# Kernel optimization log

Hardware: AMD Instinct MI355X
Metric: run time of the kernel (lower is better)

## Reference

```python
import jax, jax.numpy as jnp
import numpy as np

B, S, V, E, H = 1024, 64, 32, 256, 512
META = 13


def setup_inputs() -> dict:
    key = jax.random.key(0)
    ks = jax.random.split(key, 12)
    return {
        "image_representation": jax.random.normal(ks[0], (B, META), jnp.float32),
        "messages": jax.random.randint(ks[1], (B, S), 0, V),
        "embedding": jax.random.normal(ks[2], (V, E), jnp.float32) * 0.1,
        "w_ih": jax.random.normal(ks[3], (4 * H, E), jnp.float32) * 0.02,
        "w_hh": jax.random.normal(ks[4], (4 * H, H), jnp.float32) * 0.02,
        "b_ih": jnp.zeros((4 * H,), jnp.float32),
        "b_hh": jnp.zeros((4 * H,), jnp.float32).at[H:2 * H].set(1.0),
        "proc_w": jax.random.normal(ks[5], (H, META), jnp.float32) * 0.1,
        "proc_b": jnp.zeros((H,), jnp.float32),
        "w1": jax.random.normal(ks[6], (H, 2 * H), jnp.float32) * 0.02,
        "b1": jnp.zeros((H,), jnp.float32),
        "w2": jax.random.normal(ks[7], (2, H), jnp.float32) * 0.02,
        "b2": jnp.zeros((2,), jnp.float32),
    }


def _lstm_run(emb_tbe, w_ih, w_hh, b_ih, b_hh):
    # emb_tbe: [S, B, E]; PyTorch LSTMCell gate order: i, f, g, o
    Bn = emb_tbe.shape[1]
    Hn = w_hh.shape[1]

    def step(carry, x_t):
        h, c = carry
        gates = x_t @ w_ih.T + b_ih + h @ w_hh.T + b_hh  # [B, 4H]
        i, f, g, o = jnp.split(gates, 4, axis=-1)
        c = jax.nn.sigmoid(f) * c + jax.nn.sigmoid(i) * jnp.tanh(g)
        h = jax.nn.sigmoid(o) * jnp.tanh(c)
        return (h, c), None

    init = (jnp.zeros((Bn, Hn), emb_tbe.dtype), jnp.zeros((Bn, Hn), emb_tbe.dtype))
    (h, _), _ = jax.lax.scan(step, init, emb_tbe)
    return h


def reference(image_representation, messages, embedding, w_ih, w_hh, b_ih, b_hh,
              proc_w, proc_b, w1, b1, w2, b2):
    emb = embedding[messages]                       # [B, S, E]
    h = _lstm_run(jnp.transpose(emb, (1, 0, 2)), w_ih, w_hh, b_ih, b_hh)  # [B, H]
    img = image_representation @ proc_w.T + proc_b  # [B, H]
    combined = jnp.concatenate([h, img], axis=1)    # [B, 2H]
    hidden = jax.nn.relu(combined @ w1.T + b1)
    prediction = hidden @ w2.T + b2                 # [B, 2]
    return prediction, emb
```

## Files before the change

kernel.cpp:

```cpp
#include <hip/hip_runtime.h>

typedef __attribute__((ext_vector_type(8))) short bf16x8;
typedef __attribute__((ext_vector_type(4))) float f32x4;
typedef unsigned long long u64;

__device__ __forceinline__ unsigned short f2bf(float x) {
    union { float f; unsigned u; } c; c.f = x;
    unsigned u = c.u + 0x7fffu + ((c.u >> 16) & 1u);
    return (unsigned short)(u >> 16);
}
__device__ __forceinline__ unsigned pack2(float a, float b) {
    return (unsigned)f2bf(a) | ((unsigned)f2bf(b) << 16);
}
__device__ __forceinline__ float sigm(float x) { return 1.f / (1.f + __expf(-x)); }
__device__ __forceinline__ float tanh_(float x) { return 1.f - 2.f / (__expf(2.f * x) + 1.f); }

#define ALOAD(p)     __hip_atomic_load((p), __ATOMIC_RELAXED, __HIP_MEMORY_SCOPE_AGENT)
#define ASTORE(p, v) __hip_atomic_store((p), (v), __ATOMIC_RELAXED, __HIP_MEMORY_SCOPE_AGENT)

__global__ __launch_bounds__(256) void prep_k(
    const float* __restrict__ emb, const float* __restrict__ w_ih,
    const float* __restrict__ b_ih, const float* __restrict__ b_hh,
    const float* __restrict__ w_hh, const float* __restrict__ w1,
    const float* __restrict__ imgr, const float* __restrict__ procw,
    const float* __restrict__ procb,
    float* __restrict__ table, unsigned short* __restrict__ Wp,
    unsigned short* __restrict__ w1p, unsigned short* __restrict__ imgb)
{
    int wg = blockIdx.x, tid = threadIdx.x;
    if (wg < 256) {
        int id = wg * 256 + tid;
        int v = id >> 11, c = id & 2047;
        int c7 = c & 127, tt = c >> 7;
        int srow = ((c7 >> 4) & 3) * 512 + tt * 32 + ((c7 >> 6) & 1) * 16 + (c7 & 15);
        const float4* e4 = (const float4*)(emb + v * 256);
        const float4* w4 = (const float4*)(w_ih + srow * 256);
        float a = 0.f;
        #pragma unroll 8
        for (int k = 0; k < 64; ++k) {
            float4 x = e4[k], y = w4[k];
            a += x.x * y.x + x.y * y.y + x.z * y.z + x.w * y.w;
        }
        table[id] = a + b_ih[srow] + b_hh[srow];
    } else if (wg < 768) {
        int id = (wg - 256) * 256 + tid;
        int c = id >> 6, j = id & 63;
        int c7 = c & 127, tt = c >> 7;
        int srow = ((c7 >> 4) & 3) * 512 + tt * 32 + ((c7 >> 6) & 1) * 16 + (c7 & 15);
        const float4* s4 = (const float4*)(w_hh + srow * 512 + j * 8);
        float4 x = s4[0], y = s4[1];
        uint4 r;
        r.x = pack2(x.x, x.y); r.y = pack2(x.z, x.w);
        r.z = pack2(y.x, y.y); r.w = pack2(y.z, y.w);
        *(uint4*)(Wp + c * 512 + j * 8) = r;
    } else if (wg < 1024) {
        int id = (wg - 768) * 256 + tid;
        const float4* s4 = (const float4*)(w1 + id * 8);
        float4 x = s4[0], y = s4[1];
        uint4 r;
        r.x = pack2(x.x, x.y); r.y = pack2(x.z, x.w);
        r.z = pack2(y.x, y.y); r.w = pack2(y.z, y.w);
        *(uint4*)(w1p + id * 8) = r;
    } else {
        int id = (wg - 1024) * 256 + tid;
        int b = id >> 9, h = id & 511;
        const float* ir = imgr + b * 13;
        const float* pw = procw + h * 13;
        float a = procb[h];
        #pragma unroll
        for (int k = 0; k < 13; ++k) a += ir[k] * pw[k];
        imgb[id] = f2bf(a);
    }
}

template<int FAST>
__device__ __forceinline__ void steps_loop(
    const uint4* BshF, const float* Tsh, const unsigned char* Msh,
    unsigned short* Hsh, u64* hb, unsigned* myflag, int g, int t)
{
    const int tid = threadIdx.x;
    const int lane = tid & 63, wid = tid >> 6;
    const int wr = wid >> 1, wc = wid & 1;
    const int l15 = lane & 15, l4 = lane >> 4;
    const int arow = g * 64 + wr * 16 + l15;
    const int bbase = wc * 4096;
    float creg[4] = {0.f, 0.f, 0.f, 0.f};

    for (int s = 0; s < 64; ++s) {
        f32x4 acc[4] = {};
        if (s > 0) {
            const unsigned tgt = (unsigned)s;
            if (FAST) {
                if (wid == 0) {
                    for (;;) {
                        unsigned v = ALOAD(&myflag[l15]);
                        if (__all((int)(v >= tgt))) break;
                    }
                }
                __syncthreads();
            } else {
                for (;;) {
                    unsigned v = ALOAD(&myflag[l15]);
                    if (__all((int)(v >= tgt))) break;
                    __builtin_amdgcn_s_sleep(1);
                }
                asm volatile("" ::: "memory");
            }
            if (FAST) {
                const uint4* hp4 = (const uint4*)(hb + (size_t)((s - 1) & 7) * 131072);
                uint4 A[16];
                #pragma unroll
                for (int kg = 0; kg < 16; ++kg)
                    A[kg] = hp4[arow * 64 + kg * 4 + l4];
                #pragma unroll
                for (int kg = 0; kg < 16; ++kg) {
                    #pragma unroll
                    for (int cf = 0; cf < 4; ++cf) {
                        bf16x8 bfr = *(const bf16x8*)&BshF[bbase + (kg * 4 + cf) * 64 + lane];
                        acc[cf] = __builtin_amdgcn_mfma_f32_16x16x32_bf16(
                            *(const bf16x8*)&A[kg], bfr, acc[cf], 0, 0, 0);
                    }
                }
            } else {
                const u64* hp = hb + (size_t)((s - 1) & 7) * 131072;
                u64 a0[16], a1[16];
                #pragma unroll
                for (int kg = 0; kg < 16; ++kg) {
                    int idx = arow * 128 + kg * 8 + l4 * 2;
                    a0[kg] = ALOAD(&hp[idx]); a1[kg] = ALOAD(&hp[idx + 1]);
                }
                #pragma unroll
                for (int kg = 0; kg < 16; ++kg) {
                    union { u64 u[2]; bf16x8 v; } A;
                    A.u[0] = a0[kg]; A.u[1] = a1[kg];
                    #pragma unroll
                    for (int cf = 0; cf < 4; ++cf) {
                        bf16x8 bfr = *(const bf16x8*)&BshF[bbase + (kg * 4 + cf) * 64 + lane];
                        acc[cf] = __builtin_amdgcn_mfma_f32_16x16x32_bf16(
                            A.v, bfr, acc[cf], 0, 0, 0);
                    }
                }
            }
        }
        #pragma unroll
        for (int reg = 0; reg < 4; ++reg) {
            int bl = wr * 16 + l4 * 4 + reg;
            int v = Msh[s * 64 + bl];
            const float* tr = Tsh + v * 128 + wc * 64 + l15;
            float gi = acc[0][reg] + tr[0];
            float gf = acc[1][reg] + tr[16];
            float gg = acc[2][reg] + tr[32];
            float go = acc[3][reg] + tr[48];
            float cn = sigm(gf) * creg[reg] + sigm(gi) * tanh_(gg);
            creg[reg] = cn;
            Hsh[bl * 40 + wc * 16 + l15] = f2bf(sigm(go) * tanh_(cn));
        }
        __syncthreads();
        {
            int row = tid >> 3, j = tid & 7;
            u64 val = *(const u64*)&Hsh[row * 40 + j * 4];
            u64* hw = hb + (size_t)(s & 7) * 131072;
            if (FAST) hw[(g * 64 + row) * 128 + t * 8 + j] = val;
            else      ASTORE(&hw[(g * 64 + row) * 128 + t * 8 + j], val);
        }
        __syncthreads();
        if (tid == 0) ASTORE(&myflag[t], (unsigned)(s + 1));
    }
}

__global__ __launch_bounds__(512, 2) void lstm_k(
    const float* __restrict__ table, const unsigned short* __restrict__ Wp,
    const int* __restrict__ msgs, u64* __restrict__ hb,
    unsigned* __restrict__ flags)
{
    extern __shared__ char smem[];
    uint4* BshF = (uint4*)smem;
    float* Tsh  = (float*)(smem + 131072);
    unsigned char* Msh = (unsigned char*)(smem + 147456);
    unsigned short* Hsh = (unsigned short*)(smem + 151552);

    const int tid = threadIdx.x;
    const int x = blockIdx.x;
    const int g = (x & 7) | (((x >> 7) & 1) << 3);
    const int t = (x >> 3) & 15;

    const uint4* wg4 = (const uint4*)Wp;
    #pragma unroll
    for (int it = 0; it < 16; ++it) {
        int p = it * 512 + tid;
        int col = p >> 6, ks = p & 63;
        uint4 v = wg4[(t * 128 + col) * 64 + ks];
        int dst = (((col >> 6) * 16 + (ks >> 2)) * 4 + ((col >> 4) & 3)) * 64
                  + (ks & 3) * 16 + (col & 15);
        BshF[dst] = v;
    }
    const uint4* tg = (const uint4*)table;
    uint4* T4 = (uint4*)Tsh;
    #pragma unroll
    for (int it = 0; it < 2; ++it) {
        int p = it * 512 + tid;
        T4[p] = tg[(p >> 5) * 512 + t * 32 + (p & 31)];
    }
    #pragma unroll
    for (int it = 0; it < 8; ++it) {
        int p = it * 512 + tid;
        int row = p >> 6, s_ = p & 63;
        Msh[s_ * 64 + row] = (unsigned char)msgs[(g * 64 + row) * 64 + s_];
    }
    __syncthreads();

    unsigned* xslots = flags + 256;
    unsigned* verd   = flags + 512;
    volatile unsigned* bc = (volatile unsigned*)Hsh;
    if (tid == 0) {
        unsigned xcd;
        asm volatile("s_getreg_b32 %0, hwreg(HW_REG_XCC_ID)" : "=s"(xcd));
        ASTORE(&xslots[g * 16 + t], xcd + 1u);
        if (t == 0) {
            unsigned ok = 1, first = 0;
            long spins = 0;
            for (int i = 0; i < 16 && ok; ++i) {
                unsigned v;
                for (;;) {
                    v = ALOAD(&xslots[g * 16 + i]);
                    if (v) break;
                    if (++spins > (1 << 20)) { ok = 0; break; }
                    __builtin_amdgcn_s_sleep(2);
                }
                if (!ok) break;
                if (i == 0) first = v;
                else if (v != first) ok = 0;
            }
            ASTORE(&verd[g], ok + 1u);
        }
        unsigned v;
        do {
            v = ALOAD(&verd[g]);
            if (!v) __builtin_amdgcn_s_sleep(2);
        } while (!v);
        bc[0] = v - 1;
    }
    __syncthreads();
    unsigned fastu = bc[0];
    __syncthreads();

    unsigned* myflag = flags + g * 16;
    if (fastu) steps_loop<1>(BshF, Tsh, Msh, Hsh, hb, myflag, g, t);
    else       steps_loop<0>(BshF, Tsh, Msh, Hsh, hb, myflag, g, t);
}

__global__ __launch_bounds__(256) void mlp2_k(
    const u64* __restrict__ hfin, const unsigned short* __restrict__ imgb,
    const unsigned short* __restrict__ w1p, const float* __restrict__ b1,
    float* __restrict__ hid)
{
    __shared__ uint4 ldsA[512];
    __shared__ uint4 ldsB[256];
    const int tid = threadIdx.x;
    const int lane = tid & 63, wid = tid >> 6;
    const int l15 = lane & 15, l4 = lane >> 4;
    const int mbase = blockIdx.y * 64;
    const int t = blockIdx.x;

    const uint4* h4 = (const uint4*)hfin;
    const uint4* ia = (const uint4*)imgb;
    const uint4* wb = (const uint4*)w1p;

    f32x4 acc[2] = {};
    uint4 ra[2], rb1;

    #pragma unroll
    for (int j = 0; j < 2; ++j) {
        int p = tid + j * 256, row = p >> 3, ss = (p & 7) ^ (row & 7);
        ra[j] = h4[(mbase + row) * 64 + ss];
    }
    {
        int col = tid >> 3, ss = (tid & 7) ^ (col & 7);
        rb1 = wb[(t * 32 + col) * 128 + ss];
    }
    #pragma unroll
    for (int j = 0; j < 2; ++j) ldsA[tid + j * 256] = ra[j];
    ldsB[tid] = rb1;
    __syncthreads();

    for (int kc = 0; kc < 16; ++kc) {
        if (kc < 15) {
            int kn = kc + 1;
            #pragma unroll
            for (int j = 0; j < 2; ++j) {
                int p = tid + j * 256, row = p >> 3, ss = (p & 7) ^ (row & 7);
                ra[j] = (kn < 8) ? h4[(mbase + row) * 64 + kn * 8 + ss]
                                 : ia[(mbase + row) * 64 + (kn - 8) * 8 + ss];
            }
            int col = tid >> 3, ss = (tid & 7) ^ (col & 7);
            rb1 = wb[(t * 32 + col) * 128 + kn * 8 + ss];
        }
        #pragma unroll
        for (int kg = 0; kg < 2; ++kg) {
            int row = wid * 16 + l15;
            bf16x8 af = *(const bf16x8*)&ldsA[row * 8 + ((kg * 4 + l4) ^ (row & 7))];
            #pragma unroll
            for (int cf = 0; cf < 2; ++cf) {
                int col = cf * 16 + l15;
                bf16x8 bf = *(const bf16x8*)&ldsB[col * 8 + ((kg * 4 + l4) ^ (col & 7))];
                acc[cf] = __builtin_amdgcn_mfma_f32_16x16x32_bf16(af, bf, acc[cf], 0, 0, 0);
            }
        }
        if (kc < 15) {
            __syncthreads();
            #pragma unroll
            for (int j = 0; j < 2; ++j) ldsA[tid + j * 256] = ra[j];
            ldsB[tid] = rb1;
            __syncthreads();
        }
    }

    #pragma unroll
    for (int reg = 0; reg < 4; ++reg) {
        int b = mbase + wid * 16 + l4 * 4 + reg;
        #pragma unroll
        for (int cf = 0; cf < 2; ++cf) {
            int n = t * 32 + cf * 16 + l15;
            hid[b * 512 + n] = fmaxf(acc[cf][reg] + b1[n], 0.f);
        }
    }
}

__global__ __launch_bounds__(256) void pred2_k(
    const float* __restrict__ hid, const float* __restrict__ w2,
    const float* __restrict__ b2, float* __restrict__ out)
{
    int wid = threadIdx.x >> 6, lane = threadIdx.x & 63;
    int b = blockIdx.x * 4 + wid;
    const float4* hr = (const float4*)(hid + b * 512);
    const float4* wA = (const float4*)(w2);
    const float4* wB = (const float4*)(w2 + 512);
    float a0 = 0.f, a1 = 0.f;
    #pragma unroll
    for (int j = 0; j < 2; ++j) {
        float4 h4 = hr[lane * 2 + j];
        float4 x0 = wA[lane * 2 + j], x1 = wB[lane * 2 + j];
        a0 += h4.x * x0.x + h4.y * x0.y + h4.z * x0.z + h4.w * x0.w;
        a1 += h4.x * x1.x + h4.y * x1.y + h4.z * x1.z + h4.w * x1.w;
    }
    #pragma unroll
    for (int off = 32; off > 0; off >>= 1) {
        a0 += __shfl_xor(a0, off);
        a1 += __shfl_xor(a1, off);
    }
    if (lane == 0) {
        out[b * 2]     = a0 + b2[0];
        out[b * 2 + 1] = a1 + b2[1];
    }
}

__global__ __launch_bounds__(256) void gather_k(
    const float* __restrict__ emb, const int* __restrict__ msgs,
    float* __restrict__ out)
{
    const float4* e4 = (const float4*)emb;
    float4* o4 = (float4*)out;
    int id = blockIdx.x * 256 + threadIdx.x;
    #pragma unroll
    for (int it = 0; it < 4; ++it) {
        int p = id + it * 1048576;
        int bs = p >> 6, e = p & 63;
        int v = msgs[bs];
        o4[p] = e4[v * 64 + e];
    }
}

extern "C" void kernel_launch(void* const* d_in, const int* in_sizes, int n_in,
                              void* d_out, int out_size, void* d_ws, size_t ws_size,
                              hipStream_t stream)
{
    const float* imgr  = (const float*)d_in[0];
    const int*   msgs  = (const int*)d_in[1];
    const float* emb   = (const float*)d_in[2];
    const float* w_ih  = (const float*)d_in[3];
    const float* w_hh  = (const float*)d_in[4];
    const float* b_ih  = (const float*)d_in[5];
    const float* b_hh  = (const float*)d_in[6];
    const float* procw = (const float*)d_in[7];
    const float* procb = (const float*)d_in[8];
    const float* w1    = (const float*)d_in[9];
    const float* b1    = (const float*)d_in[10];
    const float* w2    = (const float*)d_in[11];
    const float* b2    = (const float*)d_in[12];
    float* outp = (float*)d_out;

    const size_t OFF_WP   = 262144;
    const size_t OFF_H    = 2359296;
    const size_t OFF_IMGB = OFF_H + 8388608;
    const size_t OFF_W1P  = OFF_IMGB + 1048576;
    const size_t OFF_HID  = OFF_W1P + 1048576;
    const size_t OFF_FLG  = OFF_HID + 2097152;
    const size_t NEED     = OFF_FLG + 4096;
    char* ws = (ws_size >= NEED) ? (char*)d_ws : (char*)(outp + 2048);

    float*          table = (float*)(ws);
    unsigned short* Wp    = (unsigned short*)(ws + OFF_WP);
    u64*            hb    = (u64*)(ws + OFF_H);
    unsigned short* imgb  = (unsigned short*)(ws + OFF_IMGB);
    unsigned short* w1p   = (unsigned short*)(ws + OFF_W1P);
    float*          hid   = (float*)(ws + OFF_HID);
    unsigned*       flags = (unsigned*)(ws + OFF_FLG);

    hipMemsetAsync(flags, 0, 4096, stream);
    hipFuncSetAttribute((const void*)lstm_k,
                        hipFuncAttributeMaxDynamicSharedMemorySize, 156672);

    prep_k<<<3072, 256, 0, stream>>>(emb, w_ih, b_ih, b_hh, w_hh, w1, imgr,
                                     procw, procb, table, Wp, w1p, imgb);
    lstm_k<<<256, 512, 156672, stream>>>(table, Wp, msgs, hb, flags);
    mlp2_k<<<dim3(16, 16), 256, 0, stream>>>(hb + (size_t)7 * 131072, imgb,
                                             w1p, b1, hid);
    pred2_k<<<256, 256, 0, stream>>>(hid, w2, b2, outp);
    gather_k<<<4096, 256, 0, stream>>>(emb, msgs, outp + 2048);
}
```

Measured before the change: 454.9 us.

## Consume peer hidden-state chunks as their flags arrive instead of waiting for all

Each LSTM block used to wait until all 16 peer blocks had published their hidden-state slice before running the recurrent matmul. Now it starts with its own slice, polls the peer flags, and runs MFMAs for each slice as soon as it is ready, so synchronization latency overlaps with compute. Hidden outputs are written straight to global memory as 16-bit stores (sc1 on the slow path), which removes the LDS staging buffer and one barrier. Flags are padded to separate 128-byte lines to cut contention. The cost is many narrow global stores and a more complex polling loop that can spin harder.

```diff
diff --git a/kernel.cpp b/kernel.cpp
--- a/kernel.cpp
+++ b/kernel.cpp
@@ -17,6 +17,11 @@
 
 #define ALOAD(p)     __hip_atomic_load((p), __ATOMIC_RELAXED, __HIP_MEMORY_SCOPE_AGENT)
 #define ASTORE(p, v) __hip_atomic_store((p), (v), __ATOMIC_RELAXED, __HIP_MEMORY_SCOPE_AGENT)
+
+__device__ __forceinline__ void st16_sc1(unsigned short* p, unsigned short v) {
+    unsigned x = v;
+    asm volatile("global_store_short %0, %1, off sc1" :: "v"(p), "v"(x) : "memory");
+}
 
 __global__ __launch_bounds__(256) void prep_k(
     const float* __restrict__ emb, const float* __restrict__ w_ih,
@@ -76,7 +81,7 @@
 template<int FAST>
 __device__ __forceinline__ void steps_loop(
     const uint4* BshF, const float* Tsh, const unsigned char* Msh,
-    unsigned short* Hsh, u64* hb, unsigned* myflag, int g, int t)
+    u64* hb, unsigned* flags_g, int g, int t)
 {
     const int tid = threadIdx.x;
     const int lane = tid & 63, wid = tid >> 6;
@@ -90,58 +95,84 @@
         f32x4 acc[4] = {};
         if (s > 0) {
             const unsigned tgt = (unsigned)s;
-            if (FAST) {
-                if (wid == 0) {
-                    for (;;) {
-                        unsigned v = ALOAD(&myflag[l15]);
-                        if (__all((int)(v >= tgt))) break;
-                    }
-                }
-                __syncthreads();
-            } else {
-                for (;;) {
-                    unsigned v = ALOAD(&myflag[l15]);
-                    if (__all((int)(v >= tgt))) break;
-                    __builtin_amdgcn_s_sleep(1);
-                }
-                asm volatile("" ::: "memory");
-            }
-            if (FAST) {
-                const uint4* hp4 = (const uint4*)(hb + (size_t)((s - 1) & 7) * 131072);
-                uint4 A[16];
-                #pragma unroll
-                for (int kg = 0; kg < 16; ++kg)
-                    A[kg] = hp4[arow * 64 + kg * 4 + l4];
-                #pragma unroll
-                for (int kg = 0; kg < 16; ++kg) {
-                    #pragma unroll
-                    for (int cf = 0; cf < 4; ++cf) {
-                        bf16x8 bfr = *(const bf16x8*)&BshF[bbase + (kg * 4 + cf) * 64 + lane];
-                        acc[cf] = __builtin_amdgcn_mfma_f32_16x16x32_bf16(
-                            *(const bf16x8*)&A[kg], bfr, acc[cf], 0, 0, 0);
-                    }
-                }
-            } else {
-                const u64* hp = hb + (size_t)((s - 1) & 7) * 131072;
-                u64 a0[16], a1[16];
-                #pragma unroll
-                for (int kg = 0; kg < 16; ++kg) {
-                    int idx = arow * 128 + kg * 8 + l4 * 2;
-                    a0[kg] = ALOAD(&hp[idx]); a1[kg] = ALOAD(&hp[idx + 1]);
+            const uint4* hp4 = (const uint4*)(hb + (size_t)((s - 1) & 7) * 131072);
+            const u64*  hp8 = hb + (size_t)((s - 1) & 7) * 131072;
+
+            {
+                bf16x8 Af;
+                if (FAST) {
+                    uint4 a = hp4[arow * 64 + t * 4 + l4];
+                    Af = *(const bf16x8*)&a;
+                } else {
+                    union { u64 u[2]; bf16x8 v; } A;
+                    int idx = arow * 128 + t * 8 + l4 * 2;
+                    A.u[0] = ALOAD(&hp8[idx]); A.u[1] = ALOAD(&hp8[idx + 1]);
+                    Af = A.v;
                 }
                 #pragma unroll
-                for (int kg = 0; kg < 16; ++kg) {
-                    union { u64 u[2]; bf16x8 v; } A;
-                    A.u[0] = a0[kg]; A.u[1] = a1[kg];
-                    #pragma unroll
-                    for (int cf = 0; cf < 4; ++cf) {
-                        bf16x8 bfr = *(const bf16x8*)&BshF[bbase + (kg * 4 + cf) * 64 + lane];
-                        acc[cf] = __builtin_amdgcn_mfma_f32_16x16x32_bf16(
-                            A.v, bfr, acc[cf], 0, 0, 0);
-                    }
+                for (int cf = 0; cf < 4; ++cf) {
+                    bf16x8 bfr = *(const bf16x8*)&BshF[bbase + (t * 4 + cf) * 64 + lane];
+                    acc[cf] = __builtin_amdgcn_mfma_f32_16x16x32_bf16(Af, bfr, acc[cf], 0, 0, 0);
                 }
             }
-        }
+            unsigned done = 1u << t;
+
+            while (done != 0xFFFFu) {
+                unsigned vv = ALOAD(&flags_g[(lane & 15) * 32]);
+                unsigned rdy = (unsigned)__ballot((int)(vv >= tgt)) & 0xFFFFu;
+                unsigned todo = rdy & ~done;
+                if (!todo) continue;
+                asm volatile("" ::: "memory");
+                if ((todo | done) == 0xFFFFu) {
+                    uint4 A[16];
+                    #pragma unroll
+                    for (int p = 0; p < 16; ++p)
+                        if (!((done >> p) & 1)) {
+                            if (FAST) A[p] = hp4[arow * 64 + p * 4 + l4];
+                            else {
+                                u64 q0 = ALOAD(&hp8[arow * 128 + p * 8 + l4 * 2]);
+                                u64 q1 = ALOAD(&hp8[arow * 128 + p * 8 + l4 * 2 + 1]);
+                                A[p] = make_uint4((unsigned)q0, (unsigned)(q0 >> 32),
+                                                  (unsigned)q1, (unsigned)(q1 >> 32));
+                            }
+                        }
+                    #pragma unroll
+                    for (int p = 0; p < 16; ++p)
+                        if (!((done >> p) & 1)) {
+                            #pragma unroll
+                            for (int cf = 0; cf < 4; ++cf) {
+                                bf16x8 bfr = *(const bf16x8*)&BshF[bbase + (p * 4 + cf) * 64 + lane];
+                                acc[cf] = __builtin_amdgcn_mfma_f32_16x16x32_bf16(
+                                    *(const bf16x8*)&A[p], bfr, acc[cf], 0, 0, 0);
+                            }
+                        }
+                    done = 0xFFFFu;
+                } else {
+                    unsigned m = todo;
+                    while (m) {
+                        int p = __ffs(m) - 1; m &= m - 1;
+                        bf16x8 Af;
+                        if (FAST) {
+                            uint4 a = hp4[arow * 64 + p * 4 + l4];
+                            Af = *(const bf16x8*)&a;
+                        } else {
+                            union { u64 u[2]; bf16x8 v; } A;
+                            int idx = arow * 128 + p * 8 + l4 * 2;
+                            A.u[0] = ALOAD(&hp8[idx]); A.u[1] = ALOAD(&hp8[idx + 1]);
+                            Af = A.v;
+                        }
+                        #pragma unroll
+                        for (int cf = 0; cf < 4; ++cf) {
+                            bf16x8 bfr = *(const bf16x8*)&BshF[bbase + (p * 4 + cf) * 64 + lane];
+                            acc[cf] = __builtin_amdgcn_mfma_f32_16x16x32_bf16(Af, bfr, acc[cf], 0, 0, 0);
+                        }
+                    }
+                    done |= todo;
+                }
+            }
+        }
+        unsigned short* hw = (unsigned short*)(hb + (size_t)(s & 7) * 131072);
+        const int U = t * 32 + wc * 16 + l15;
         #pragma unroll
         for (int reg = 0; reg < 4; ++reg) {
             int bl = wr * 16 + l4 * 4 + reg;
@@ -153,18 +184,12 @@
             float go = acc[3][reg] + tr[48];
             float cn = sigm(gf) * creg[reg] + sigm(gi) * tanh_(gg);
             creg[reg] = cn;
-            Hsh[bl * 40 + wc * 16 + l15] = f2bf(sigm(go) * tanh_(cn));
+            unsigned short hv = f2bf(sigm(go) * tanh_(cn));
+            if (FAST) hw[(g * 64 + bl) * 512 + U] = hv;
+            else      st16_sc1(&hw[(g * 64 + bl) * 512 + U], hv);
         }
         __syncthreads();
-        {
-            int row = tid >> 3, j = tid & 7;
-            u64 val = *(const u64*)&Hsh[row * 40 + j * 4];
-            u64* hw = hb + (size_t)(s & 7) * 131072;
-            if (FAST) hw[(g * 64 + row) * 128 + t * 8 + j] = val;
-            else      ASTORE(&hw[(g * 64 + row) * 128 + t * 8 + j], val);
-        }
-        __syncthreads();
-        if (tid == 0) ASTORE(&myflag[t], (unsigned)(s + 1));
+        if (tid == 0) ASTORE(&flags_g[t * 32], (unsigned)(s + 1));
     }
 }
 
@@ -177,7 +202,7 @@
     uint4* BshF = (uint4*)smem;
     float* Tsh  = (float*)(smem + 131072);
     unsigned char* Msh = (unsigned char*)(smem + 147456);
-    unsigned short* Hsh = (unsigned short*)(smem + 151552);
+    volatile unsigned* bc = (volatile unsigned*)(smem + 151552);
 
     const int tid = threadIdx.x;
     const int x = blockIdx.x;
@@ -209,9 +234,8 @@
     }
     __syncthreads();
 
-    unsigned* xslots = flags + 256;
-    unsigned* verd   = flags + 512;
-    volatile unsigned* bc = (volatile unsigned*)Hsh;
+    unsigned* xslots = flags + 8192;
+    unsigned* verd   = flags + 8448;
     if (tid == 0) {
         unsigned xcd;
         asm volatile("s_getreg_b32 %0, hwreg(HW_REG_XCC_ID)" : "=s"(xcd));
@@ -244,9 +268,9 @@
     unsigned fastu = bc[0];
     __syncthreads();
 
-    unsigned* myflag = flags + g * 16;
-    if (fastu) steps_loop<1>(BshF, Tsh, Msh, Hsh, hb, myflag, g, t);
-    else       steps_loop<0>(BshF, Tsh, Msh, Hsh, hb, myflag, g, t);
+    unsigned* flags_g = flags + g * 512;
+    if (fastu) steps_loop<1>(BshF, Tsh, Msh, hb, flags_g, g, t);
+    else       steps_loop<0>(BshF, Tsh, Msh, hb, flags_g, g, t);
 }
 
 __global__ __launch_bounds__(256) void mlp2_k(
@@ -395,7 +419,7 @@
     const size_t OFF_W1P  = OFF_IMGB + 1048576;
     const size_t OFF_HID  = OFF_W1P + 1048576;
     const size_t OFF_FLG  = OFF_HID + 2097152;
-    const size_t NEED     = OFF_FLG + 4096;
+    const size_t NEED     = OFF_FLG + 36864;
     char* ws = (ws_size >= NEED) ? (char*)d_ws : (char*)(outp + 2048);
 
     float*          table = (float*)(ws);
@@ -406,7 +430,7 @@
     float*          hid   = (float*)(ws + OFF_HID);
     unsigned*       flags = (unsigned*)(ws + OFF_FLG);
 
-    hipMemsetAsync(flags, 0, 4096, stream);
+    hipMemsetAsync(flags, 0, 36864, stream);
     hipFuncSetAttribute((const void*)lstm_k,
                         hipFuncAttributeMaxDynamicSharedMemorySize, 156672);
 
```

Result: slower. 493.3 us (+8.4%).
